# Kernel optimization log

Hardware: AMD Instinct MI355X
Metric: run time of the kernel (lower is better)

## Reference

```python
import jax, jax.numpy as jnp
import numpy as np

N_ATOMS = 2_000_000
N_FEAT = 64
NUM_GRAPHS = 16384


def setup_inputs() -> dict:
    key = jax.random.key(0)
    k1, k2 = jax.random.split(key)
    atom_features = jax.random.normal(k1, (N_ATOMS, N_FEAT), dtype=jnp.float32)
    node_graph_indices = jnp.sort(
        jax.random.randint(k2, (N_ATOMS,), 0, NUM_GRAPHS, dtype=jnp.int32)
    )
    return {
        "atom_features": atom_features,
        "node_graph_indices": node_graph_indices,
        "num_graphs": NUM_GRAPHS,
    }


def reference(atom_features, node_graph_indices, num_graphs):
    # Per-graph softmax (note: TF original uses raw exp, no max-subtraction)
    exp_state = jnp.exp(atom_features)  # (N_atoms, F)
    denom = jax.ops.segment_sum(exp_state, node_graph_indices,
                                num_segments=num_graphs)  # (G, F)
    softmaxed = exp_state / denom[node_graph_indices]  # (N_atoms, F)
    weighted = atom_features * softmaxed
    # Weighted segment-sum -> per-graph readout, shape (G, F)
    return jax.ops.segment_sum(weighted, node_graph_indices,
                               num_segments=num_graphs)
```

## Files before the change

### kernel.cpp

```cpp
#include <hip/hip_runtime.h>


__device__ __forceinline__ int lower_bound_i32(const int* __restrict__ idx,
                                               int n, int target) {
    int lo = 0, hi = n;
    while (lo < hi) {
        int mid = (lo + hi) >> 1;
        if (idx[mid] < target) lo = mid + 1;
        else hi = mid;
    }
    return lo;
}

__global__ __launch_bounds__(256) void readout_kernel(
    const float* __restrict__ x,
    const int* __restrict__ gidx,
    float* __restrict__ out,
    int n_atoms, int num_graphs)
{
    const int wave = threadIdx.x >> 6;
    const int g = blockIdx.x * 4 + wave;
    if (g >= num_graphs) return;

    const int lane = threadIdx.x & 63;
    const int r = lane >> 4;
    const int q = lane & 15;

    const int start = lower_bound_i32(gidx, n_atoms, g);
    const int end   = lower_bound_i32(gidx, n_atoms, g + 1);

    const float4* __restrict__ xq = (const float4*)x;

    float4 num = make_float4(0.f, 0.f, 0.f, 0.f);
    float4 den = make_float4(0.f, 0.f, 0.f, 0.f);

    for (int a = start + r; a < end; a += 4) {
        float4 v = xq[(size_t)a * 16 + q];
        float4 e;
        e.x = __expf(v.x);
        e.y = __expf(v.y);
        e.z = __expf(v.z);
        e.w = __expf(v.w);
        den.x += e.x;          den.y += e.y;
        den.z += e.z;          den.w += e.w;
        num.x += v.x * e.x;    num.y += v.y * e.y;
        num.z += v.z * e.z;    num.w += v.w * e.w;
    }

    #pragma unroll
    for (int off = 16; off <= 32; off <<= 1) {
        num.x += __shfl_xor(num.x, off);
        num.y += __shfl_xor(num.y, off);
        num.z += __shfl_xor(num.z, off);
        num.w += __shfl_xor(num.w, off);
        den.x += __shfl_xor(den.x, off);
        den.y += __shfl_xor(den.y, off);
        den.z += __shfl_xor(den.z, off);
        den.w += __shfl_xor(den.w, off);
    }

    if (r == 0) {
        float4 o;
        o.x = (den.x != 0.f) ? num.x / den.x : 0.f;
        o.y = (den.y != 0.f) ? num.y / den.y : 0.f;
        o.z = (den.z != 0.f) ? num.z / den.z : 0.f;
        o.w = (den.w != 0.f) ? num.w / den.w : 0.f;
        ((float4*)out)[(size_t)g * 16 + q] = o;
    }
}

extern "C" void kernel_launch(void* const* d_in, const int* in_sizes, int n_in,
                              void* d_out, int out_size, void* d_ws, size_t ws_size,
                              hipStream_t stream) {
    const float* x    = (const float*)d_in[0];
    const int*   gidx = (const int*)d_in[1];
    float*       out  = (float*)d_out;

    const int n_atoms    = in_sizes[1];
    const int num_graphs = out_size / 64;

    const int blocks = (num_graphs + 3) / 4;
    readout_kernel<<<blocks, 256, 0, stream>>>(x, gidx, out, n_atoms, num_graphs);
}
```

Measured before the change: 678.4 us.

## Precompute segment offsets and unroll atom loop with nontemporal loads

```diff
diff --git a/kernel.cpp b/kernel.cpp
--- a/kernel.cpp
+++ b/kernel.cpp
@@ -1,22 +1,37 @@
 #include <hip/hip_runtime.h>
 
 
-__device__ __forceinline__ int lower_bound_i32(const int* __restrict__ idx,
-                                               int n, int target) {
-    int lo = 0, hi = n;
-    while (lo < hi) {
-        int mid = (lo + hi) >> 1;
-        if (idx[mid] < target) lo = mid + 1;
-        else hi = mid;
+typedef float f4 __attribute__((ext_vector_type(4)));
+
+__global__ __launch_bounds__(256) void offsets_kernel(
+    const int* __restrict__ gidx, int* __restrict__ starts,
+    int n_atoms, int num_graphs)
+{
+    int i = blockIdx.x * blockDim.x + threadIdx.x;
+    if (i >= n_atoms) return;
+    if (i == 0) {
+        int b = gidx[0];
+        for (int g = 0; g <= b && g < num_graphs; ++g) starts[g] = 0;
+        starts[num_graphs] = n_atoms;
+    } else {
+        int a = gidx[i - 1];
+        int b = gidx[i];
+        for (int g = a + 1; g <= b && g < num_graphs; ++g) starts[g] = i;
     }
-    return lo;
+}
+
+__device__ __forceinline__ void accum(f4 v, f4& num, f4& den) {
+    f4 e;
+    e.x = __expf(v.x); e.y = __expf(v.y); e.z = __expf(v.z); e.w = __expf(v.w);
+    den += e;
+    num += v * e;
 }
 
 __global__ __launch_bounds__(256) void readout_kernel(
     const float* __restrict__ x,
-    const int* __restrict__ gidx,
+    const int* __restrict__ starts,
     float* __restrict__ out,
-    int n_atoms, int num_graphs)
+    int num_graphs)
 {
     const int wave = threadIdx.x >> 6;
     const int g = blockIdx.x * 4 + wave;
@@ -26,26 +41,42 @@
     const int r = lane >> 4;
     const int q = lane & 15;
 
-    const int start = lower_bound_i32(gidx, n_atoms, g);
-    const int end   = lower_bound_i32(gidx, n_atoms, g + 1);
+    const int start = starts[g];
+    const int end   = starts[g + 1];
 
-    const float4* __restrict__ xq = (const float4*)x;
+    const f4* __restrict__ xq = (const f4*)x;
 
-    float4 num = make_float4(0.f, 0.f, 0.f, 0.f);
-    float4 den = make_float4(0.f, 0.f, 0.f, 0.f);
+    f4 z = {0.f, 0.f, 0.f, 0.f};
+    f4 num0 = z, den0 = z, num1 = z, den1 = z;
+    f4 num2 = z, den2 = z, num3 = z, den3 = z;
 
-    for (int a = start + r; a < end; a += 4) {
-        float4 v = xq[(size_t)a * 16 + q];
-        float4 e;
-        e.x = __expf(v.x);
-        e.y = __expf(v.y);
-        e.z = __expf(v.z);
-        e.w = __expf(v.w);
-        den.x += e.x;          den.y += e.y;
-        den.z += e.z;          den.w += e.w;
-        num.x += v.x * e.x;    num.y += v.y * e.y;
-        num.z += v.z * e.z;    num.w += v.w * e.w;
+    int a = start + r;
+    for (; a + 28 < end; a += 32) {
+        f4 v0 = __builtin_nontemporal_load(&xq[(size_t)(a     ) * 16 + q]);
+        f4 v1 = __builtin_nontemporal_load(&xq[(size_t)(a +  4) * 16 + q]);
+        f4 v2 = __builtin_nontemporal_load(&xq[(size_t)(a +  8) * 16 + q]);
+        f4 v3 = __builtin_nontemporal_load(&xq[(size_t)(a + 12) * 16 + q]);
+        f4 v4 = __builtin_nontemporal_load(&xq[(size_t)(a + 16) * 16 + q]);
+        f4 v5 = __builtin_nontemporal_load(&xq[(size_t)(a + 20) * 16 + q]);
+        f4 v6 = __builtin_nontemporal_load(&xq[(size_t)(a + 24) * 16 + q]);
+        f4 v7 = __builtin_nontemporal_load(&xq[(size_t)(a + 28) * 16 + q]);
+        accum(v0, num0, den0); accum(v1, num1, den1);
+        accum(v2, num2, den2); accum(v3, num3, den3);
+        accum(v4, num0, den0); accum(v5, num1, den1);
+        accum(v6, num2, den2); accum(v7, num3, den3);
     }
+    for (; a + 4 < end; a += 8) {
+        f4 v0 = __builtin_nontemporal_load(&xq[(size_t)(a    ) * 16 + q]);
+        f4 v1 = __builtin_nontemporal_load(&xq[(size_t)(a + 4) * 16 + q]);
+        accum(v0, num0, den0); accum(v1, num1, den1);
+    }
+    for (; a < end; a += 4) {
+        f4 v = __builtin_nontemporal_load(&xq[(size_t)a * 16 + q]);
+        accum(v, num2, den2);
+    }
+
+    f4 num = (num0 + num1) + (num2 + num3);
+    f4 den = (den0 + den1) + (den2 + den3);
 
     #pragma unroll
     for (int off = 16; off <= 32; off <<= 1) {
@@ -60,12 +91,12 @@
     }
 
     if (r == 0) {
-        float4 o;
+        f4 o;
         o.x = (den.x != 0.f) ? num.x / den.x : 0.f;
         o.y = (den.y != 0.f) ? num.y / den.y : 0.f;
         o.z = (den.z != 0.f) ? num.z / den.z : 0.f;
         o.w = (den.w != 0.f) ? num.w / den.w : 0.f;
-        ((float4*)out)[(size_t)g * 16 + q] = o;
+        ((f4*)out)[(size_t)g * 16 + q] = o;
     }
 }
 
@@ -75,10 +106,14 @@
     const float* x    = (const float*)d_in[0];
     const int*   gidx = (const int*)d_in[1];
     float*       out  = (float*)d_out;
+    int*         starts = (int*)d_ws;
 
     const int n_atoms    = in_sizes[1];
     const int num_graphs = out_size / 64;
 
-    const int blocks = (num_graphs + 3) / 4;
-    readout_kernel<<<blocks, 256, 0, stream>>>(x, gidx, out, n_atoms, num_graphs);
+    const int blocks1 = (n_atoms + 255) / 256;
+    offsets_kernel<<<blocks1, 256, 0, stream>>>(gidx, starts, n_atoms, num_graphs);
+
+    const int blocks2 = (num_graphs + 3) / 4;
+    readout_kernel<<<blocks2, 256, 0, stream>>>(x, starts, out, num_graphs);
 }
```

Measured after the change: 628.9 us. 1.08x faster.
